# Kernel optimization log

Measured on AMD Instinct MI355X. Metric: run time of the kernel, lower is better.

The kernel has to match this reference:

```python
import jax, jax.numpy as jnp
import numpy as np

# static config (matches init_kwargs)
PL, LAT, LON = 8, 48, 96
WP, WL, WW = 2, 6, 12
SP, SL, SN = 1, 3, 6
NH = 16


def _earth_position_index(ws):
    wp, wl, ww = ws
    zi = np.arange(wp); zj = -np.arange(wp) * wp
    hi = np.arange(wl); hj = -np.arange(wl) * wl
    w = np.arange(ww)
    c1 = np.stack(np.meshgrid(zi, hi, w, indexing='ij')).reshape(3, -1)
    c2 = np.stack(np.meshgrid(zj, hj, w, indexing='ij')).reshape(3, -1)
    coords = (c1[:, :, None] - c2[:, None, :]).transpose(1, 2, 0).astype(np.int64)
    coords[:, :, 2] += ww - 1
    coords[:, :, 1] *= 2 * ww - 1
    coords[:, :, 0] *= (2 * ww - 1) * wl * wl
    return coords.sum(-1)  # (N, N)

_POS_IDX = jnp.asarray(_earth_position_index((WP, WL, WW)))


def _ln(x, w, b, eps=1e-5):
    m = x.mean(-1, keepdims=True)
    v = x.var(-1, keepdims=True)
    return (x - m) / jnp.sqrt(v + eps) * w + b


def setup_inputs() -> dict:
    key = jax.random.key(0)
    ks = jax.random.split(key, 8)
    B, C = 1, 512
    L = PL * LAT * LON
    TOW = (PL // WP) * (LAT // WL)
    TBL = WP * WP * WL * WL * (2 * WW - 1)
    s = 0.02
    return {
        'x': jax.random.normal(ks[0], (B, L, C), jnp.float32),
        'norm1_w': jnp.ones((C,), jnp.float32), 'norm1_b': jnp.zeros((C,), jnp.float32),
        'qkv_w': jax.random.normal(ks[1], (C, 3 * C), jnp.float32) * s,
        'qkv_b': jnp.zeros((3 * C,), jnp.float32),
        'proj_w': jax.random.normal(ks[2], (C, C), jnp.float32) * s,
        'proj_b': jnp.zeros((C,), jnp.float32),
        'bias_table': jax.random.normal(ks[3], (TBL, TOW, NH), jnp.float32) * s,
        'norm2_w': jnp.ones((C,), jnp.float32), 'norm2_b': jnp.zeros((C,), jnp.float32),
        'mlp_w1': jax.random.normal(ks[4], (C, 4 * C), jnp.float32) * s,
        'mlp_b1': jnp.zeros((4 * C,), jnp.float32),
        'mlp_w2': jax.random.normal(ks[5], (4 * C, C), jnp.float32) * s,
        'mlp_b2': jnp.zeros((C,), jnp.float32),
    }


def reference(x, norm1_w, norm1_b, qkv_w, qkv_b, proj_w, proj_b, bias_table,
              norm2_w, norm2_b, mlp_w1, mlp_b1, mlp_w2, mlp_b2):
    B, L, C = x.shape
    HD = C // NH
    scale = HD ** -0.5
    N = WP * WL * WW
    nPl, nLat, nLon = PL // WP, LAT // WL, LON // WW
    nW = nPl * nLat

    # norm1 + roll + window partition (B, nLon, nPl, nLat, wp, wl, ww, C)
    h = _ln(x, norm1_w, norm1_b).reshape(B, PL, LAT, LON, C)
    h = jnp.roll(h, (-SP, -SL, -SN), axis=(1, 2, 3))
    h = h.reshape(B, nPl, WP, nLat, WL, nLon, WW, C)
    h = h.transpose(0, 5, 1, 3, 2, 4, 6, 7).reshape(B * nLon, nW, N, C)

    # attention
    qkv = (h @ qkv_w + qkv_b).reshape(B * nLon, nW, N, 3, NH, HD)
    qkv = qkv.transpose(3, 0, 4, 1, 2, 5)  # (3, B_, nh, nW, N, hd)
    q, k, v = qkv[0] * scale, qkv[1], qkv[2]
    attn = jnp.einsum('bhwnd,bhwmd->bhwnm', q, k)
    bias = bias_table[_POS_IDX.reshape(-1)].reshape(N, N, nW, NH)
    bias = bias.transpose(3, 2, 0, 1)  # (nh, nW, N, N)
    attn = jax.nn.softmax(attn + bias[None], axis=-1)
    o = jnp.einsum('bhwnm,bhwmd->bhwnd', attn, v)
    o = o.transpose(0, 2, 3, 1, 4).reshape(B * nLon, nW, N, C)
    o = o @ proj_w + proj_b

    # reverse partition + roll back
    o = o.reshape(B, nLon, nPl, nLat, WP, WL, WW, C)
    o = o.transpose(0, 2, 4, 3, 5, 1, 6, 7).reshape(B, PL, LAT, LON, C)
    o = jnp.roll(o, (SP, SL, SN), axis=(1, 2, 3)).reshape(B, L, C)

    x = x + o
    h2 = _ln(x, norm2_w, norm2_b)
    h2 = jax.nn.gelu(h2 @ mlp_w1 + mlp_b1, approximate=False) @ mlp_w2 + mlp_b2
    return x + h2
```

## Files before the change

### kernel.cpp

```cpp
#include <hip/hip_runtime.h>
#include <hip/hip_bf16.h>
#include <math.h>

typedef __bf16 bf16;
typedef __attribute__((ext_vector_type(8))) __bf16 bf16x8;
typedef __attribute__((ext_vector_type(4))) float f32x4;
typedef __attribute__((ext_vector_type(8))) float f32x8;

#define NTOK   36864
#define CDIM   512
#define NHEAD  16
#define HD     32
#define NWIN   32
#define NLON   8
#define WTOK   144
#define TBL    3312

#define GLOAD_LDS16(g, l) __builtin_amdgcn_global_load_lds( \
    (const __attribute__((address_space(1))) void*)(const void*)(g), \
    (__attribute__((address_space(3))) void*)(l), 16, 0, 0)

__device__ __forceinline__ int src_token(int r) {
    int ww_ = r % 12; int q = r / 12;
    int wl_ = q % 6;  q /= 6;
    int wp_ = q & 1;  q >>= 1;
    int lat_g = q & 7; q >>= 3;
    int pl_g = q & 3;  q >>= 2;
    int lon_g = q;
    int pl  = pl_g * 2 + wp_ + 1;  if (pl  >= 8)  pl  -= 8;
    int lat = lat_g * 6 + wl_ + 3; if (lat >= 48) lat -= 48;
    int lon = lon_g * 12 + ww_ + 6; if (lon >= 96) lon -= 96;
    return (pl * 48 + lat) * 96 + lon;
}

__device__ __forceinline__ float gelu_exact(float x) {
    return 0.5f * x * (1.0f + erff(x * 0.70710678118654752f));
}

__global__ __launch_bounds__(256) void transpose_weights(const float* __restrict__ qkv_w,
                                                         const float* __restrict__ proj_w,
                                                         const float* __restrict__ w1,
                                                         const float* __restrict__ w2,
                                                         bf16* __restrict__ wtq,
                                                         bf16* __restrict__ wtp,
                                                         bf16* __restrict__ wt1,
                                                         bf16* __restrict__ wt2) {
    __shared__ bf16 tile[32][33];
    int bid = blockIdx.x;
    const float* in; bf16* outp; int R, Cc, ti;
    if (bid < 768)       { in = qkv_w;  outp = wtq; R = 512;  Cc = 1536; ti = bid; }
    else if (bid < 1024) { in = proj_w; outp = wtp; R = 512;  Cc = 512;  ti = bid - 768; }
    else if (bid < 2048) { in = w1;     outp = wt1; R = 512;  Cc = 2048; ti = bid - 1024; }
    else                 { in = w2;     outp = wt2; R = 2048; Cc = 512;  ti = bid - 2048; }
    int gx = Cc >> 5;
    int c0 = (ti % gx) * 32, r0 = (ti / gx) * 32;
    int tx = threadIdx.x & 31, ty = threadIdx.x >> 5;
#pragma unroll
    for (int i = 0; i < 32; i += 8)
        tile[ty + i][tx] = (bf16)in[(size_t)(r0 + ty + i) * Cc + c0 + tx];
    __syncthreads();
#pragma unroll
    for (int i = 0; i < 32; i += 8)
        outp[(size_t)(c0 + ty + i) * R + r0 + tx] = tile[tx][ty + i];
}

__global__ __launch_bounds__(256) void table_transpose(const float* __restrict__ in,
                                                       float* __restrict__ outT) {
    __shared__ float tile[32][33];
    int i0 = blockIdx.x * 32, w0 = blockIdx.y * 32;
    int tx = threadIdx.x & 31, ty = threadIdx.x >> 5;
#pragma unroll
    for (int r = 0; r < 32; r += 8)
        if (i0 + ty + r < TBL) tile[ty + r][tx] = in[(size_t)(i0 + ty + r) * 512 + w0 + tx];
    __syncthreads();
#pragma unroll
    for (int r = 0; r < 32; r += 8)
        if (i0 + tx < TBL) outT[(size_t)(w0 + ty + r) * TBL + i0 + tx] = tile[tx][ty + r];
}

template<bool PERM>
__global__ __launch_bounds__(256) void ln_kernel(const float* __restrict__ in,
                                                 const float* __restrict__ w,
                                                 const float* __restrict__ b,
                                                 bf16* __restrict__ out) {
    int r = blockIdx.x * 4 + (threadIdx.x >> 6);
    int lane = threadIdx.x & 63;
    int s = PERM ? src_token(r) : r;
    f32x8 v8 = *(const f32x8*)(in + (size_t)s * CDIM + lane * 8);
    float sum = 0.f, sq = 0.f;
#pragma unroll
    for (int i = 0; i < 8; ++i) { sum += v8[i]; sq += v8[i] * v8[i]; }
#pragma unroll
    for (int m = 1; m < 64; m <<= 1) { sum += __shfl_xor(sum, m); sq += __shfl_xor(sq, m); }
    float mean = sum * (1.f / 512.f);
    float var  = sq  * (1.f / 512.f) - mean * mean;
    float rstd = rsqrtf(var + 1e-5f);
    f32x8 w8 = *(const f32x8*)(w + lane * 8);
    f32x8 b8 = *(const f32x8*)(b + lane * 8);
    bf16x8 o8;
#pragma unroll
    for (int i = 0; i < 8; ++i)
        o8[i] = (bf16)((v8[i] - mean) * rstd * w8[i] + b8[i]);
    *(bf16x8*)(out + (size_t)r * CDIM + lane * 8) = o8;
}

template<int EPI>
__global__ __launch_bounds__(256) void gemm_bt(const bf16* __restrict__ A,
                                               const bf16* __restrict__ Bt,
                                               const float* __restrict__ bias,
                                               void* __restrict__ Cout_,
                                               const float* __restrict__ X,
                                               int K, int N, int gx) {
    __shared__ bf16 As[2 * 128 * 32];
    __shared__ bf16 Bs[2 * 128 * 32];
    int t = threadIdx.x;
    int wid = t >> 6, lane = t & 63;
    int wr = wid >> 1, wc = wid & 1;
    int g = lane >> 4, cl = lane & 15;

    int nwg = gridDim.x, orig = blockIdx.x;
    int wg = orig;
    if ((nwg & 7) == 0) {
        int cpx = nwg >> 3;
        wg = (orig & 7) * cpx + (orig >> 3);
    }
    int m0 = (wg / gx) * 128, n0 = (wg % gx) * 128;
    f32x4 acc[4][4] = {};

    int srow = wid * 16 + (lane >> 2);
    int scol = (lane & 3) * 8;
    const bf16* Ag0 = A  + (size_t)(m0 + srow) * K + scol;
    const bf16* Ag1 = Ag0 + (size_t)64 * K;
    const bf16* Bg0 = Bt + (size_t)(n0 + srow) * K + scol;
    const bf16* Bg1 = Bg0 + (size_t)64 * K;
    int ldsoff = wid * 16 * 32;

    GLOAD_LDS16(Ag0, As + ldsoff);
    GLOAD_LDS16(Ag1, As + 64 * 32 + ldsoff);
    GLOAD_LDS16(Bg0, Bs + ldsoff);
    GLOAD_LDS16(Bg1, Bs + 64 * 32 + ldsoff);
    __syncthreads();

    int nt = K >> 5, cur = 0;
    for (int kt = 0; kt < nt; ++kt) {
        if (kt + 1 < nt) {
            int k1 = (kt + 1) << 5;
            bf16* Ad = As + (cur ^ 1) * 4096;
            bf16* Bd = Bs + (cur ^ 1) * 4096;
            GLOAD_LDS16(Ag0 + k1, Ad + ldsoff);
            GLOAD_LDS16(Ag1 + k1, Ad + 64 * 32 + ldsoff);
            GLOAD_LDS16(Bg0 + k1, Bd + ldsoff);
            GLOAD_LDS16(Bg1 + k1, Bd + 64 * 32 + ldsoff);
        }
        const bf16* Ar = As + cur * 4096;
        const bf16* Br = Bs + cur * 4096;
        bf16x8 af[4], bfv[4];
#pragma unroll
        for (int i = 0; i < 4; ++i)
            af[i]  = *(const bf16x8*)(Ar + (wr * 64 + i * 16 + cl) * 32 + g * 8);
#pragma unroll
        for (int i = 0; i < 4; ++i)
            bfv[i] = *(const bf16x8*)(Br + (wc * 64 + i * 16 + cl) * 32 + g * 8);
#pragma unroll
        for (int mi = 0; mi < 4; ++mi)
#pragma unroll
            for (int ni = 0; ni < 4; ++ni)
                acc[mi][ni] = __builtin_amdgcn_mfma_f32_16x16x32_bf16(af[mi], bfv[ni], acc[mi][ni], 0, 0, 0);
        __syncthreads();
        cur ^= 1;
    }

#pragma unroll
    for (int mi = 0; mi < 4; ++mi) {
#pragma unroll
        for (int j = 0; j < 4; ++j) {
            int row = m0 + wr * 64 + mi * 16 + g * 4 + j;
            int srw = 0;
            if (EPI == 2) srw = src_token(row);
#pragma unroll
            for (int ni = 0; ni < 4; ++ni) {
                int col = n0 + wc * 64 + ni * 16 + cl;
                float v = acc[mi][ni][j] + bias[col];
                if (EPI == 1) v = gelu_exact(v);
                if (EPI == 0 || EPI == 1) {
                    ((bf16*)Cout_)[(size_t)row * N + col] = (bf16)v;
                } else if (EPI == 2) {
                    size_t o = (size_t)srw * CDIM + col;
                    ((float*)Cout_)[o] = X[o] + v;
                } else {
                    size_t o = (size_t)row * N + col;
                    ((float*)Cout_)[o] += v;
                }
            }
        }
    }
}

__global__ __launch_bounds__(256) void attn_mfma(const bf16* __restrict__ qkv,
                                                 const float* __restrict__ tableT,
                                                 bf16* __restrict__ obuf) {
    int wgs = (blockIdx.x & 7) * 512 + (blockIdx.x >> 3);
    int h  = wgs & 15;
    int w  = (wgs >> 4) & 31;
    int b_ = wgs >> 9;
    int t = threadIdx.x, wid = t >> 6, lane = t & 63;
    int g = lane >> 4, cl = lane & 15;
    size_t base = ((size_t)b_ * NWIN + w) * WTOK;

    __shared__ bf16 P[WTOK * 168];
    __shared__ bf16 vT[32 * 168];
    __shared__ float bias_s[TBL];
    bf16* qs = P;
    bf16* ks = P + WTOK * 40;

    const bf16* qg = qkv + base * 1536 + h * 32;
    for (int tok = t >> 2; tok < WTOK; tok += 64) {
        int c8 = (t & 3) * 8;
        *(bf16x8*)(qs + tok * 40 + c8) = *(const bf16x8*)(qg + (size_t)tok * 1536 + c8);
        *(bf16x8*)(ks + tok * 40 + c8) = *(const bf16x8*)(qg + 512 + (size_t)tok * 1536 + c8);
        bf16x8 v8 = *(const bf16x8*)(qg + 1024 + (size_t)tok * 1536 + c8);
#pragma unroll
        for (int i = 0; i < 8; ++i) vT[(c8 + i) * 168 + tok] = v8[i];
    }
    for (int z = t; z < 32 * 24; z += 256) vT[(z / 24) * 168 + 144 + (z % 24)] = (bf16)0.f;
    const float* tb = tableT + (size_t)(w * 16 + h) * TBL;
    for (int i = t; i < TBL; i += 256) bias_s[i] = tb[i];
    __syncthreads();

    f32x4 sacc[3][9] = {};
    bf16x8 kf[9];
#pragma unroll
    for (int ct = 0; ct < 9; ++ct)
        kf[ct] = *(const bf16x8*)(ks + (ct * 16 + cl) * 40 + g * 8);
#pragma unroll
    for (int rti = 0; rti < 3; ++rti) {
        int rt = wid + rti * 4;
        if (rt < 9) {
            bf16x8 qf = *(const bf16x8*)(qs + (rt * 16 + cl) * 40 + g * 8);
#pragma unroll
            for (int ct = 0; ct < 9; ++ct)
                sacc[rti][ct] = __builtin_amdgcn_mfma_f32_16x16x32_bf16(qf, kf[ct], sacc[rti][ct], 0, 0, 0);
        }
    }
    __syncthreads();

    for (int z = t; z < WTOK * 24; z += 256) P[(z / 24) * 168 + 144 + (z % 24)] = (bf16)0.f;

    int bm[9];
#pragma unroll
    for (int ct = 0; ct < 9; ++ct) {
        int m = ct * 16 + cl;
        int wm = m % 12, tm = m / 12, hm = tm % 6, zm = tm / 6;
        bm[ct] = zm * 1656 + hm * 138 + 11 - wm;
    }

    const float scale = 0.17677669529663689f;
    float rinv[3][4];
#pragma unroll
    for (int rti = 0; rti < 3; ++rti) {
        int rt = wid + rti * 4;
        if (rt < 9) {
#pragma unroll
            for (int j = 0; j < 4; ++j) {
                int row = rt * 16 + g * 4 + j;
                int wn = row % 12, tn = row / 12, hn = tn % 6, zn = tn / 6;
                int an = zn * 828 + hn * 23 + wn;
                float mx = -1e30f;
#pragma unroll
                for (int ct = 0; ct < 9; ++ct) {
                    float v = sacc[rti][ct][j] * scale + bias_s[an + bm[ct]];
                    sacc[rti][ct][j] = v;
                    mx = fmaxf(mx, v);
                }
                for (int msk = 1; msk < 16; msk <<= 1) mx = fmaxf(mx, __shfl_xor(mx, msk));
                float sm = 0.f;
#pragma unroll
                for (int ct = 0; ct < 9; ++ct) {
                    float p = __expf(sacc[rti][ct][j] - mx);
                    sm += p;
                    P[row * 168 + ct * 16 + cl] = (bf16)p;
                }
                for (int msk = 1; msk < 16; msk <<= 1) sm += __shfl_xor(sm, msk);
                rinv[rti][j] = 1.f / sm;
            }
        }
    }
    __syncthreads();

#pragma unroll
    for (int rti = 0; rti < 3; ++rti) {
        int rt = wid + rti * 4;
        if (rt < 9) {
            f32x4 oacc[2] = {};
#pragma unroll
            for (int ks_ = 0; ks_ < 5; ++ks_) {
                bf16x8 pf = *(const bf16x8*)(P + (rt * 16 + cl) * 168 + ks_ * 32 + g * 8);
#pragma unroll
                for (int c2 = 0; c2 < 2; ++c2) {
                    bf16x8 vf = *(const bf16x8*)(vT + (c2 * 16 + cl) * 168 + ks_ * 32 + g * 8);
                    oacc[c2] = __builtin_amdgcn_mfma_f32_16x16x32_bf16(pf, vf, oacc[c2], 0, 0, 0);
                }
            }
#pragma unroll
            for (int c2 = 0; c2 < 2; ++c2)
#pragma unroll
                for (int j = 0; j < 4; ++j) {
                    int row = rt * 16 + g * 4 + j;
                    obuf[(base + row) * CDIM + h * 32 + c2 * 16 + cl] =
                        (bf16)(oacc[c2][j] * rinv[rti][j]);
                }
        }
    }
}

extern "C" void kernel_launch(void* const* d_in, const int* in_sizes, int n_in,
                              void* d_out, int out_size, void* d_ws, size_t ws_size,
                              hipStream_t stream) {
    const float* x       = (const float*)d_in[0];
    const float* n1w     = (const float*)d_in[1];
    const float* n1b     = (const float*)d_in[2];
    const float* qkv_w   = (const float*)d_in[3];
    const float* qkv_b   = (const float*)d_in[4];
    const float* proj_w  = (const float*)d_in[5];
    const float* proj_b  = (const float*)d_in[6];
    const float* btab    = (const float*)d_in[7];
    const float* n2w     = (const float*)d_in[8];
    const float* n2b     = (const float*)d_in[9];
    const float* mlp_w1  = (const float*)d_in[10];
    const float* mlp_b1  = (const float*)d_in[11];
    const float* mlp_w2  = (const float*)d_in[12];
    const float* mlp_b2  = (const float*)d_in[13];
    float* out = (float*)d_out;

    const size_t OFF_HBUF = 0;
    const size_t OFF_QKV  = 37748736;
    const size_t OFF_TT   = 150994944;
    const size_t OFF_OBUF = 188743680;
    const size_t OFF_WTQ  = 226492416;
    const size_t OFF_WTP  = 228065280;
    const size_t OFF_WT1  = 228589568;
    const size_t OFF_WT2  = 230686720;
    const size_t NEED     = 232783872;

    if (ws_size < NEED) return;

    char* ws = (char*)d_ws;
    bf16*  hbuf   = (bf16*)(ws + OFF_HBUF);
    bf16*  qkvbuf = (bf16*)(ws + OFF_QKV);
    bf16*  midbuf = qkvbuf;
    float* tableT = (float*)(ws + OFF_TT);
    bf16*  obuf   = (bf16*)(ws + OFF_OBUF);
    bf16*  wtq    = (bf16*)(ws + OFF_WTQ);
    bf16*  wtp    = (bf16*)(ws + OFF_WTP);
    bf16*  wt1    = (bf16*)(ws + OFF_WT1);
    bf16*  wt2    = (bf16*)(ws + OFF_WT2);

    transpose_weights<<<3072, 256, 0, stream>>>(qkv_w, proj_w, mlp_w1, mlp_w2,
                                                wtq, wtp, wt1, wt2);
    table_transpose<<<dim3((TBL + 31) / 32, 512 / 32), 256, 0, stream>>>(btab, tableT);

    ln_kernel<true><<<NTOK / 4, 256, 0, stream>>>(x, n1w, n1b, hbuf);

    gemm_bt<0><<<12 * 288, 256, 0, stream>>>(hbuf, wtq, qkv_b, qkvbuf, nullptr, 512, 1536, 12);

    attn_mfma<<<4096, 256, 0, stream>>>(qkvbuf, tableT, obuf);

    gemm_bt<2><<<4 * 288, 256, 0, stream>>>(obuf, wtp, proj_b, out, x, 512, 512, 4);

    ln_kernel<false><<<NTOK / 4, 256, 0, stream>>>(out, n2w, n2b, hbuf);

    gemm_bt<1><<<16 * 288, 256, 0, stream>>>(hbuf, wt1, mlp_b1, midbuf, nullptr, 512, 2048, 16);

    gemm_bt<3><<<4 * 288, 256, 0, stream>>>(midbuf, wt2, mlp_b2, out, nullptr, 2048, 512, 4);
}
```

Before: 571.1 us.

## Add 256x256-tile triple-buffered GEMM kernel for QKV and MLP-up projections

Introduces a new 512-thread GEMM kernel with 256x256 output tiles, a three-stage LDS ring filled by direct global-to-LDS loads, split MFMA phases with raised wave priority, and a cross-XCD workgroup remap. It replaces the 128-tile gemm_bt for the QKV and first MLP GEMMs. The bf16 store epilogue is removed from gemm_bt, since only the proj and MLP-down variants still use it. Larger tiles raise operand reuse and cut global traffic per FLOP, at the cost of higher register pressure and fewer workgroups.

```diff
diff --git a/kernel.cpp b/kernel.cpp
--- a/kernel.cpp
+++ b/kernel.cpp
@@ -181,16 +181,107 @@
             for (int ni = 0; ni < 4; ++ni) {
                 int col = n0 + wc * 64 + ni * 16 + cl;
                 float v = acc[mi][ni][j] + bias[col];
-                if (EPI == 1) v = gelu_exact(v);
-                if (EPI == 0 || EPI == 1) {
-                    ((bf16*)Cout_)[(size_t)row * N + col] = (bf16)v;
-                } else if (EPI == 2) {
+                if (EPI == 2) {
                     size_t o = (size_t)srw * CDIM + col;
                     ((float*)Cout_)[o] = X[o] + v;
                 } else {
                     size_t o = (size_t)row * N + col;
                     ((float*)Cout_)[o] += v;
                 }
+            }
+        }
+    }
+}
+
+template<int EPI>
+__global__ __launch_bounds__(512, 2) void gemm256(const bf16* __restrict__ A,
+                                                  const bf16* __restrict__ Bt,
+                                                  const float* __restrict__ bias,
+                                                  bf16* __restrict__ Cout,
+                                                  int K, int N, int gx) {
+    __shared__ char lds[3 * 32768];
+    const int t = threadIdx.x;
+    const int wid = t >> 6, lane = t & 63;
+    const int wr = wid >> 2, wc = wid & 3;
+    const int g = lane >> 4, cl = lane & 15;
+
+    int nwg = gridDim.x, orig = blockIdx.x;
+    int cpx = nwg >> 3;
+    int wg = (orig & 7) * cpx + (orig >> 3);
+    const int m0 = (wg / gx) * 256, n0 = (wg % gx) * 256;
+
+    f32x4 acc[8][4] = {};
+
+    const bf16* sbase = (wid < 4) ? A : Bt;
+    const int soff0 = (wid < 4) ? m0 : n0;
+    const int fr0 = (wid & 3) * 4;
+    const int adst = (wid >= 4) ? 16384 : 0;
+
+#define STAGE256(kt, buf) do {                                                        \
+        int kk = (kt) << 5;                                                           \
+        char* bb = lds + (buf) * 32768 + adst;                                        \
+        _Pragma("unroll")                                                             \
+        for (int c = 0; c < 4; ++c) {                                                 \
+            const bf16* src = sbase + (size_t)(soff0 + (fr0 + c) * 16 + cl) * K + kk + g * 8; \
+            GLOAD_LDS16(src, bb + (fr0 + c) * 1024);                                  \
+        }                                                                             \
+    } while (0)
+
+    const int nt = K >> 5;
+    STAGE256(0, 0);
+    STAGE256(1, 1);
+    asm volatile("s_waitcnt vmcnt(4)" ::: "memory");
+    __builtin_amdgcn_s_barrier();
+
+    for (int kt = 0; kt < nt; ++kt) {
+        const char* rb = lds + (kt % 3) * 32768;
+        bf16x8 aF[4], bF[4];
+
+#pragma unroll
+        for (int j = 0; j < 4; ++j)
+            aF[j] = *(const bf16x8*)(rb + (wr * 8 + j) * 1024 + lane * 16);
+#pragma unroll
+        for (int i = 0; i < 4; ++i)
+            bF[i] = *(const bf16x8*)(rb + 16384 + (wc * 4 + i) * 1024 + lane * 16);
+        if (kt + 2 < nt) STAGE256(kt + 2, (kt + 2) % 3);
+        __builtin_amdgcn_s_barrier();
+        __builtin_amdgcn_s_setprio(1);
+#pragma unroll
+        for (int j = 0; j < 4; ++j)
+#pragma unroll
+            for (int i = 0; i < 4; ++i)
+                acc[j][i] = __builtin_amdgcn_mfma_f32_16x16x32_bf16(aF[j], bF[i], acc[j][i], 0, 0, 0);
+        __builtin_amdgcn_s_setprio(0);
+        __builtin_amdgcn_s_barrier();
+
+#pragma unroll
+        for (int j = 0; j < 4; ++j)
+            aF[j] = *(const bf16x8*)(rb + (wr * 8 + 4 + j) * 1024 + lane * 16);
+        if (kt + 2 < nt)      asm volatile("s_waitcnt vmcnt(4)" ::: "memory");
+        else if (kt + 1 < nt) asm volatile("s_waitcnt vmcnt(0)" ::: "memory");
+        __builtin_amdgcn_s_barrier();
+        __builtin_amdgcn_s_setprio(1);
+#pragma unroll
+        for (int j = 0; j < 4; ++j)
+#pragma unroll
+            for (int i = 0; i < 4; ++i)
+                acc[4 + j][i] = __builtin_amdgcn_mfma_f32_16x16x32_bf16(aF[j], bF[i], acc[4 + j][i], 0, 0, 0);
+        __builtin_amdgcn_s_setprio(0);
+        __builtin_amdgcn_s_barrier();
+    }
+#undef STAGE256
+
+#pragma unroll
+    for (int mf = 0; mf < 8; ++mf) {
+#pragma unroll
+        for (int jj = 0; jj < 4; ++jj) {
+            int row = m0 + wr * 128 + mf * 16 + g * 4 + jj;
+#pragma unroll
+            for (int nf = 0; nf < 4; ++nf) {
+                int col = n0 + wc * 64 + nf * 16 + cl;
+                float v = acc[mf][nf][jj] + bias[col];
+                if (EPI == 1) v = gelu_exact(v);
+                Cout[(size_t)row * N + col] = (bf16)v;
             }
         }
     }
@@ -361,7 +452,7 @@
 
     ln_kernel<true><<<NTOK / 4, 256, 0, stream>>>(x, n1w, n1b, hbuf);
 
-    gemm_bt<0><<<12 * 288, 256, 0, stream>>>(hbuf, wtq, qkv_b, qkvbuf, nullptr, 512, 1536, 12);
+    gemm256<0><<<144 * 6, 512, 0, stream>>>(hbuf, wtq, qkv_b, qkvbuf, 512, 1536, 6);
 
     attn_mfma<<<4096, 256, 0, stream>>>(qkvbuf, tableT, obuf);
 
@@ -369,7 +460,7 @@
 
     ln_kernel<false><<<NTOK / 4, 256, 0, stream>>>(out, n2w, n2b, hbuf);
 
-    gemm_bt<1><<<16 * 288, 256, 0, stream>>>(hbuf, wt1, mlp_b1, midbuf, nullptr, 512, 2048, 16);
+    gemm256<1><<<144 * 8, 512, 0, stream>>>(hbuf, wt1, mlp_b1, midbuf, 512, 2048, 8);
 
     gemm_bt<3><<<4 * 288, 256, 0, stream>>>(midbuf, wt2, mlp_b2, out, nullptr, 2048, 512, 4);
 }
```

Measured after the change: 604.7 us. +5.9%, slower.
